# Kernel optimization log

Hardware: AMD Instinct MI355X
Metric: run time of the kernel (lower is better)

The kernel has to match this reference:

```python
import jax, jax.numpy as jnp
import numpy as np

B, L, D = 32, 256, 512
MAX_DUR = 8.0
MAX_LEN = int(L * MAX_DUR)  # static upper bound on expanded length (round(u<8) <= 8)


def setup_inputs() -> dict:
    key = jax.random.key(0)
    k1, k2 = jax.random.split(key)
    att_out = jax.random.normal(k1, (B, L, D), dtype=jnp.float32)
    # predicted per-phoneme durations in frames (float, gets rounded inside)
    duration = jax.random.uniform(k2, (B, L), dtype=jnp.float32, minval=0.0, maxval=MAX_DUR)
    return {"att_out": att_out, "duration": duration, "alpha": 1}


def reference(att_out, duration, alpha):
    # r[b,l] = number of times phoneme l is repeated (torch.round = half-to-even, same as jnp.round)
    r = jnp.round(duration * alpha).astype(jnp.int32)                 # [B, L]
    csum = jnp.cumsum(r, axis=1)                                      # [B, L] cumulative end offsets
    total = csum[:, -1]                                               # [B] valid length per batch
    pos = jnp.arange(MAX_LEN, dtype=jnp.int32)                        # [T]
    # output frame t comes from phoneme index = first l with csum[l] > t
    idx = jax.vmap(lambda c: jnp.searchsorted(c, pos, side='right'))(csum)  # [B, T]
    idx = jnp.minimum(idx, L - 1)
    out = jnp.take_along_axis(att_out, idx[:, :, None], axis=1)       # [B, T, D] gather-expand
    mask = (pos[None, :] < total[:, None])[:, :, None]                # zero-pad like pad_sequence
    return jnp.where(mask, out, jnp.zeros((), dtype=att_out.dtype))
```

## Files before the change

kernel.cpp:

```cpp
#include <hip/hip_runtime.h>


constexpr int B = 32;
constexpr int L = 256;
constexpr int D = 512;
constexpr int MAX_LEN = 2048;
constexpr int POS_PER_BLOCK = 16;
constexpr int THREADS = 256;

__global__ __launch_bounds__(THREADS) void length_regulator_kernel(
    const float* __restrict__ att_out,
    const float* __restrict__ duration,
    const int*   __restrict__ alpha_p,
    float*       __restrict__ out)
{
    __shared__ int csum[L];

    const int b        = blockIdx.y;
    const int pos_base = blockIdx.x * POS_PER_BLOCK;
    const int tid      = threadIdx.x;

    const float alpha = (float)alpha_p[0];

    int v = (int)rintf(duration[b * L + tid] * alpha);
    csum[tid] = v;
    __syncthreads();
    #pragma unroll
    for (int off = 1; off < L; off <<= 1) {
        int add = (tid >= off) ? csum[tid - off] : 0;
        __syncthreads();
        csum[tid] += add;
        __syncthreads();
    }
    const int total = csum[L - 1];

    const int lane_in_row = tid & 127;
    const int row_in_pass = tid >> 7;

    const float4* __restrict__ src4 = (const float4*)(att_out + (size_t)b * L * D);
    float4*       __restrict__ dst4 = (float4*)(out + (size_t)b * MAX_LEN * D);

    #pragma unroll
    for (int i = 0; i < POS_PER_BLOCK; i += 2) {
        const int p = pos_base + i + row_in_pass;
        float4 val;
        if (p < total) {
            int lo = 0, hi = L;
            #pragma unroll
            while (lo < hi) {
                int mid = (lo + hi) >> 1;
                if (csum[mid] <= p) lo = mid + 1; else hi = mid;
            }
            val = src4[(size_t)lo * (D / 4) + lane_in_row];
        } else {
            val = make_float4(0.f, 0.f, 0.f, 0.f);
        }
        dst4[(size_t)p * (D / 4) + lane_in_row] = val;
    }
}

extern "C" void kernel_launch(void* const* d_in, const int* in_sizes, int n_in,
                              void* d_out, int out_size, void* d_ws, size_t ws_size,
                              hipStream_t stream) {
    const float* att_out  = (const float*)d_in[0];
    const float* duration = (const float*)d_in[1];
    const int*   alpha    = (const int*)d_in[2];
    float*       out      = (float*)d_out;

    dim3 grid(MAX_LEN / POS_PER_BLOCK, B);
    dim3 block(THREADS);
    length_regulator_kernel<<<grid, block, 0, stream>>>(att_out, duration, alpha, out);
}
```

Before: 156.4 us.

## Split index computation into separate kernel and use nontemporal stores in copy

```diff
diff --git a/kernel.cpp b/kernel.cpp
--- a/kernel.cpp
+++ b/kernel.cpp
@@ -8,18 +8,16 @@
 constexpr int POS_PER_BLOCK = 16;
 constexpr int THREADS = 256;
 
-__global__ __launch_bounds__(THREADS) void length_regulator_kernel(
-    const float* __restrict__ att_out,
+typedef float vfloat4 __attribute__((ext_vector_type(4)));
+
+__global__ __launch_bounds__(THREADS) void index_kernel(
     const float* __restrict__ duration,
     const int*   __restrict__ alpha_p,
-    float*       __restrict__ out)
+    int*         __restrict__ idx_map)
 {
     __shared__ int csum[L];
-
-    const int b        = blockIdx.y;
-    const int pos_base = blockIdx.x * POS_PER_BLOCK;
-    const int tid      = threadIdx.x;
-
+    const int b   = blockIdx.x;
+    const int tid = threadIdx.x;
     const float alpha = (float)alpha_p[0];
 
     int v = (int)rintf(duration[b * L + tid] * alpha);
@@ -34,28 +32,50 @@
     }
     const int total = csum[L - 1];
 
-    const int lane_in_row = tid & 127;
-    const int row_in_pass = tid >> 7;
-
-    const float4* __restrict__ src4 = (const float4*)(att_out + (size_t)b * L * D);
-    float4*       __restrict__ dst4 = (float4*)(out + (size_t)b * MAX_LEN * D);
-
     #pragma unroll
-    for (int i = 0; i < POS_PER_BLOCK; i += 2) {
-        const int p = pos_base + i + row_in_pass;
-        float4 val;
+    for (int j = 0; j < MAX_LEN / THREADS; ++j) {
+        const int p = tid + j * THREADS;
+        int result = -1;
         if (p < total) {
             int lo = 0, hi = L;
-            #pragma unroll
             while (lo < hi) {
                 int mid = (lo + hi) >> 1;
                 if (csum[mid] <= p) lo = mid + 1; else hi = mid;
             }
-            val = src4[(size_t)lo * (D / 4) + lane_in_row];
-        } else {
-            val = make_float4(0.f, 0.f, 0.f, 0.f);
+            result = lo;
         }
-        dst4[(size_t)p * (D / 4) + lane_in_row] = val;
+        idx_map[b * MAX_LEN + p] = result;
+    }
+}
+
+__global__ __launch_bounds__(THREADS) void copy_kernel(
+    const float* __restrict__ att_out,
+    const int*   __restrict__ idx_map,
+    float*       __restrict__ out)
+{
+    const int b        = blockIdx.y;
+    const int pos_base = blockIdx.x * POS_PER_BLOCK;
+    const int tid      = threadIdx.x;
+    const int lane     = tid & 127;
+    const int row      = tid >> 7;
+
+    const vfloat4* __restrict__ src4 = (const vfloat4*)(att_out + (size_t)b * L * D);
+    vfloat4*       __restrict__ dst4 = (vfloat4*)(out + (size_t)b * MAX_LEN * D);
+    const int*     __restrict__ im   = idx_map + b * MAX_LEN + pos_base;
+
+    int ids[POS_PER_BLOCK / 2];
+    #pragma unroll
+    for (int i = 0; i < POS_PER_BLOCK / 2; ++i)
+        ids[i] = im[2 * i + row];
+
+    #pragma unroll
+    for (int i = 0; i < POS_PER_BLOCK / 2; ++i) {
+        const int p  = pos_base + 2 * i + row;
+        const int id = ids[i];
+        vfloat4 v = (vfloat4)0.f;
+        if (id >= 0)
+            v = src4[(size_t)id * (D / 4) + lane];
+        __builtin_nontemporal_store(v, &dst4[(size_t)p * (D / 4) + lane]);
     }
 }
 
@@ -66,8 +86,10 @@
     const float* duration = (const float*)d_in[1];
     const int*   alpha    = (const int*)d_in[2];
     float*       out      = (float*)d_out;
+    int*         idx_map  = (int*)d_ws;
+
+    index_kernel<<<dim3(B), dim3(THREADS), 0, stream>>>(duration, alpha, idx_map);
 
     dim3 grid(MAX_LEN / POS_PER_BLOCK, B);
-    dim3 block(THREADS);
-    length_regulator_kernel<<<grid, block, 0, stream>>>(att_out, duration, alpha, out);
+    copy_kernel<<<grid, dim3(THREADS), 0, stream>>>(att_out, idx_map, out);
 }
```

Result: slower. 170.0 us (+8.6%).
